# Kernel optimization log

Measured on AMD Instinct MI355X. Metric: run time of the kernel, lower is better.

Reference implementation:

```python
import jax, jax.numpy as jnp
import numpy as np

N, E, H, PIN, PEIN, POUT, L = 50000, 800000, 128, 16, 8, 8, 4
EPS = 1e-7


def setup_inputs() -> dict:
    key = jax.random.key(0)
    ks = jax.random.split(key, 24)
    f = jax.random.normal
    inp = {
        'x': f(ks[0], (N, PIN), jnp.float32),
        'edge_attr': f(ks[1], (E, PEIN), jnp.float32),
        'edge_index': jax.random.randint(ks[2], (2, E), 0, N, jnp.int32),
        # encoders
        'node_W': f(ks[3], (PIN, H)) * (1.0 / np.sqrt(PIN)),
        'node_b': jnp.zeros((H,)),
        'edge_W': f(ks[4], (PEIN, H)) * (1.0 / np.sqrt(PEIN)),
        'edge_b': jnp.zeros((H,)),
        # GENConv params per layer (stacked over L): MLP Linear(H,2H)->LN->ReLU->Linear(2H,H), temp t
        'W1': f(ks[5], (L, H, 2 * H)) * (1.0 / np.sqrt(H)),
        'b1': jnp.zeros((L, 2 * H)),
        'g1': jnp.ones((L, 2 * H)),
        'be1': jnp.zeros((L, 2 * H)),
        'W2': f(ks[6], (L, 2 * H, H)) * (1.0 / np.sqrt(2 * H)),
        'b2': jnp.zeros((L, H)),
        't': jnp.ones((L,)),
        # DeepGCNLayer LayerNorms
        'ng': jnp.ones((L, H)),
        'nb': jnp.zeros((L, H)),
        # output head
        'out_W': f(ks[7], (H, POUT)) * (1.0 / np.sqrt(H)),
        'out_b': jnp.zeros((POUT,)),
    }
    return inp


def _layernorm(x, g, b):
    mu = jnp.mean(x, -1, keepdims=True)
    v = jnp.mean(jnp.square(x - mu), -1, keepdims=True)
    return (x - mu) * jax.lax.rsqrt(v + 1e-5) * g + b


def reference(x, edge_attr, edge_index, node_W, node_b, edge_W, edge_b,
              W1, b1, g1, be1, W2, b2, t, ng, nb, out_W, out_b):
    src, dst = edge_index[0], edge_index[1]

    def genconv(h, e, i):
        # message: relu(x_j + edge_attr) + eps   [E, H]
        msg = jax.nn.relu(h[src] + e) + EPS
        # softmax aggregation over edges per destination node, temperature t[i]
        s = msg * t[i]
        m = jax.ops.segment_max(s, dst, num_segments=N)  # [N, H]
        w = jnp.exp(s - m[dst])
        denom = jax.ops.segment_sum(w, dst, num_segments=N)
        agg = jax.ops.segment_sum(msg * w, dst, num_segments=N)
        agg = jnp.where(denom > 0, agg / jnp.maximum(denom, EPS), 0.0)
        # root add, then 2-layer MLP (Linear -> LN -> ReLU -> Linear)
        z = agg + h
        z = jax.nn.relu(_layernorm(z @ W1[i] + b1[i], g1[i], be1[i]))
        return z @ W2[i] + b2[i]

    h = x @ node_W + node_b                      # node encoder
    e = jax.nn.sigmoid(edge_attr @ edge_W + edge_b)  # edge encoder
    h = genconv(h, e, 0)                         # layers[0].conv only
    for i in range(1, L):                        # res+ blocks
        z = jax.nn.relu(_layernorm(h, ng[i], nb[i]))
        h = h + genconv(z, e, i)
    h = jax.nn.relu(_layernorm(h, ng[0], nb[0]))  # layers[0] norm+act; dropout=eval identity
    return h @ out_W + out_b
```

## Files before the change

### kernel.cpp

```cpp
#include <hip/hip_runtime.h>
#include <hip/hip_bf16.h>

#define NN 50000
#define NE 800000
#define HH 128
#define PIN_ 16
#define PEIN_ 8
#define POUT_ 8
#define LAYERS_ 4
#define EPSM 1e-7f

typedef __bf16 bf16x8 __attribute__((ext_vector_type(8)));
typedef float f32x4 __attribute__((ext_vector_type(4)));
typedef float f32x2 __attribute__((ext_vector_type(2)));

__device__ inline unsigned short f2bf(float f) {
  unsigned int u = __float_as_uint(f);
  u += 0x7FFFu + ((u >> 16) & 1u);
  return (unsigned short)(u >> 16);
}
__device__ inline unsigned int packbf(float lo, float hi) {
  return (unsigned int)f2bf(lo) | ((unsigned int)f2bf(hi) << 16);
}
__device__ inline float bflo(unsigned int p) { return __uint_as_float(p << 16); }
__device__ inline float bfhi(unsigned int p) { return __uint_as_float(p & 0xFFFF0000u); }
__device__ inline f32x2 unpk(unsigned int p) {
  return (f32x2){__uint_as_float(p << 16), __uint_as_float(p & 0xFFFF0000u)};
}


__global__ void count_deg_kernel(const int* __restrict__ dst, int* __restrict__ deg) {
  int i = blockIdx.x * blockDim.x + threadIdx.x;
  if (i < NE) atomicAdd(&deg[dst[i]], 1);
}

__global__ __launch_bounds__(1024) void scan_kernel(const int* __restrict__ deg,
                                                    int* __restrict__ row_ptr,
                                                    int* __restrict__ cursor, int n) {
  __shared__ int wsum[16];
  __shared__ int carry_s;
  int t = threadIdx.x;
  int lane = t & 63, wv = t >> 6;
  if (t == 0) carry_s = 0;
  __syncthreads();
  for (int base = 0; base < n; base += 1024) {
    int i = base + t;
    int v = (i < n) ? deg[i] : 0;
    int x = v;
#pragma unroll
    for (int off = 1; off < 64; off <<= 1) {
      int y = __shfl_up(x, off, 64);
      if (lane >= off) x += y;
    }
    if (lane == 63) wsum[wv] = x;
    __syncthreads();
    if (wv == 0 && lane < 16) {
      int s = wsum[lane];
#pragma unroll
      for (int off = 1; off < 16; off <<= 1) {
        int y = __shfl_up(s, off, 16);
        if (lane >= off) s += y;
      }
      wsum[lane] = s;
    }
    __syncthreads();
    int waveExcl = (wv > 0) ? wsum[wv - 1] : 0;
    int carry = carry_s;
    int excl = carry + waveExcl + x - v;
    if (i < n) { row_ptr[i] = excl; cursor[i] = excl; }
    __syncthreads();
    if (t == 1023) carry_s = carry + wsum[15];
    __syncthreads();
  }
  if (t == 0) row_ptr[n] = carry_s;
}

__global__ void scatter_kernel(const int* __restrict__ src, const int* __restrict__ dst,
                               int* __restrict__ cursor, int2* __restrict__ csr,
                               int* __restrict__ srcs) {
  int i = blockIdx.x * blockDim.x + threadIdx.x;
  if (i < NE) {
    int d = dst[i];
    int pos = atomicAdd(&cursor[d], 1);
    csr[pos] = make_int2(src[i], i);
    srcs[pos] = src[i];
  }
}


__global__ __launch_bounds__(256) void edge_enc_kernel(
    const int2* __restrict__ csr, const float* __restrict__ edge_attr,
    const float* __restrict__ edge_W, const float* __restrict__ edge_b,
    int cap, unsigned int* __restrict__ epk) {
  int wv = threadIdx.x >> 6, lane = threadIdx.x & 63;
  int p = blockIdx.x * 4 + wv;
  if (p >= cap) return;
  int2 se = csr[p];
  const float4* ea = (const float4*)(edge_attr + (size_t)se.y * PEIN_);
  float4 A = ea[0], B = ea[1];
  float acc0 = edge_b[lane], acc1 = edge_b[lane + 64];
#pragma unroll
  for (int k = 0; k < PEIN_; ++k) {
    float av = (k < 4) ? ((k == 0) ? A.x : (k == 1) ? A.y : (k == 2) ? A.z : A.w)
                       : ((k == 4) ? B.x : (k == 5) ? B.y : (k == 6) ? B.z : B.w);
    acc0 = fmaf(av, edge_W[k * HH + lane], acc0);
    acc1 = fmaf(av, edge_W[k * HH + lane + 64], acc1);
  }
  float e0 = __builtin_amdgcn_rcpf(1.f + __expf(-acc0));
  float e1 = __builtin_amdgcn_rcpf(1.f + __expf(-acc1));
  epk[(size_t)p * 64 + lane] = packbf(e0, e1);
}


__device__ __forceinline__ void estep(unsigned int ep, unsigned int zp, float t,
                                      f32x2& d, f32x2& a) {
  f32x2 msg = unpk(zp) + unpk(ep);
  msg = __builtin_elementwise_max(msg, (f32x2){0.f, 0.f});
  msg += (f32x2){EPSM, EPSM};
  f32x2 s = msg * t;
  f32x2 w;
  w.x = __expf(s.x);
  w.y = __expf(s.y);
  d += w;
  a = __builtin_elementwise_fma(msg, w, a);
}

__device__ __forceinline__ void edge_step(float4 A, float4 B, unsigned int zp,
                                          const f32x2* ew, f32x2 eb, float t,
                                          f32x2& d, f32x2& a) {
  f32x2 acc = eb;
  acc = __builtin_elementwise_fma((f32x2){A.x, A.x}, ew[0], acc);
  acc = __builtin_elementwise_fma((f32x2){A.y, A.y}, ew[1], acc);
  acc = __builtin_elementwise_fma((f32x2){A.z, A.z}, ew[2], acc);
  acc = __builtin_elementwise_fma((f32x2){A.w, A.w}, ew[3], acc);
  acc = __builtin_elementwise_fma((f32x2){B.x, B.x}, ew[4], acc);
  acc = __builtin_elementwise_fma((f32x2){B.y, B.y}, ew[5], acc);
  acc = __builtin_elementwise_fma((f32x2){B.z, B.z}, ew[6], acc);
  acc = __builtin_elementwise_fma((f32x2){B.w, B.w}, ew[7], acc);
  f32x2 e;
  e.x = __builtin_amdgcn_rcpf(1.f + __expf(-acc.x));
  e.y = __builtin_amdgcn_rcpf(1.f + __expf(-acc.y));
  f32x2 msg = unpk(zp) + e;
  msg = __builtin_elementwise_max(msg, (f32x2){0.f, 0.f});
  msg += (f32x2){EPSM, EPSM};
  f32x2 s = msg * t;
  f32x2 w;
  w.x = __expf(s.x);
  w.y = __expf(s.y);
  d += w;
  a = __builtin_elementwise_fma(msg, w, a);
}

__global__ __launch_bounds__(256) void aggregate_hyb_kernel(
    const int* __restrict__ row_ptr, const int2* __restrict__ csr,
    const int* __restrict__ srcs, const unsigned int* __restrict__ epk, int cap,
    const float* __restrict__ edge_attr, const float* __restrict__ edge_W,
    const float* __restrict__ edge_b, const unsigned int* __restrict__ zpk,
    const float* __restrict__ t_all, int layer, unsigned int* __restrict__ upk) {
  int wv = threadIdx.x >> 6, lane = threadIdx.x & 63;
  int n = blockIdx.x * 4 + wv;
  if (n >= NN) return;
  float t = t_all[layer];
  int beg = row_ptr[n], end = row_ptr[n + 1];
  unsigned int zs = zpk[(size_t)n * 64 + lane];
  f32x2 d = {0.f, 0.f}, a = {0.f, 0.f};

  if (end <= cap) {
    int p = beg;
    for (; p + 4 <= end; p += 4) {
      int s0 = srcs[p], s1 = srcs[p + 1], s2 = srcs[p + 2], s3 = srcs[p + 3];
      unsigned int e0 = epk[(size_t)(p + 0) * 64 + lane];
      unsigned int e1 = epk[(size_t)(p + 1) * 64 + lane];
      unsigned int e2 = epk[(size_t)(p + 2) * 64 + lane];
      unsigned int e3 = epk[(size_t)(p + 3) * 64 + lane];
      unsigned int z0 = zpk[(size_t)s0 * 64 + lane];
      unsigned int z1 = zpk[(size_t)s1 * 64 + lane];
      unsigned int z2 = zpk[(size_t)s2 * 64 + lane];
      unsigned int z3 = zpk[(size_t)s3 * 64 + lane];
      estep(e0, z0, t, d, a);
      estep(e1, z1, t, d, a);
      estep(e2, z2, t, d, a);
      estep(e3, z3, t, d, a);
    }
    for (; p < end; ++p) {
      unsigned int e = epk[(size_t)p * 64 + lane];
      unsigned int z = zpk[(size_t)srcs[p] * 64 + lane];
      estep(e, z, t, d, a);
    }
  } else {
    f32x2 ew[PEIN_];
#pragma unroll
    for (int k = 0; k < PEIN_; ++k)
      ew[k] = (f32x2){edge_W[k * HH + lane], edge_W[k * HH + lane + 64]};
    f32x2 eb = (f32x2){edge_b[lane], edge_b[lane + 64]};
    int p = beg;
    for (; p + 4 <= end; p += 4) {
      int2 se0 = csr[p + 0];
      int2 se1 = csr[p + 1];
      int2 se2 = csr[p + 2];
      int2 se3 = csr[p + 3];
      const float4* e0p = (const float4*)(edge_attr + (size_t)se0.y * PEIN_);
      const float4* e1p = (const float4*)(edge_attr + (size_t)se1.y * PEIN_);
      const float4* e2p = (const float4*)(edge_attr + (size_t)se2.y * PEIN_);
      const float4* e3p = (const float4*)(edge_attr + (size_t)se3.y * PEIN_);
      float4 A0 = e0p[0], B0 = e0p[1];
      float4 A1 = e1p[0], B1 = e1p[1];
      float4 A2 = e2p[0], B2 = e2p[1];
      float4 A3 = e3p[0], B3 = e3p[1];
      unsigned int z0 = zpk[(size_t)se0.x * 64 + lane];
      unsigned int z1 = zpk[(size_t)se1.x * 64 + lane];
      unsigned int z2 = zpk[(size_t)se2.x * 64 + lane];
      unsigned int z3 = zpk[(size_t)se3.x * 64 + lane];
      edge_step(A0, B0, z0, ew, eb, t, d, a);
      edge_step(A1, B1, z1, ew, eb, t, d, a);
      edge_step(A2, B2, z2, ew, eb, t, d, a);
      edge_step(A3, B3, z3, ew, eb, t, d, a);
    }
    for (; p < end; ++p) {
      int2 se = csr[p];
      const float4* ep = (const float4*)(edge_attr + (size_t)se.y * PEIN_);
      float4 A = ep[0], B = ep[1];
      unsigned int zp = zpk[(size_t)se.x * 64 + lane];
      edge_step(A, B, zp, ew, eb, t, d, a);
    }
  }

  float agg0 = (d.x > 0.f) ? a.x / fmaxf(d.x, EPSM) : 0.f;
  float agg1 = (d.y > 0.f) ? a.y / fmaxf(d.y, EPSM) : 0.f;
  upk[(size_t)n * 64 + lane] = packbf(agg0 + bflo(zs), agg1 + bfhi(zs));
}


__global__ __launch_bounds__(256) void prep_weights_kernel(
    const float* __restrict__ W1, const float* __restrict__ W2,
    unsigned short* __restrict__ W1Tp, unsigned short* __restrict__ W2T) {
  int idx = blockIdx.x * 256 + threadIdx.x;
  if (idx >= LAYERS_ * 256 * 128) return;
  int l = idx >> 15, r = idx & 32767;
  int n = r >> 7, p = r & 127;
  int k = (p >> 1) + ((p & 1) << 6);
  W1Tp[idx] = f2bf(W1[(l << 15) + k * 256 + n]);
  int c = r >> 8, kk = r & 255;
  W2T[idx] = f2bf(W2[(l << 15) + kk * 128 + c]);
}


__global__ __launch_bounds__(64) void node_enc_kernel(const float* __restrict__ x,
                                                      const float* __restrict__ W,
                                                      const float* __restrict__ b,
                                                      unsigned int* __restrict__ hbp) {
  __shared__ float xs[8 * PIN_];
  int f = threadIdx.x;
  float w0[PIN_], w1[PIN_];
#pragma unroll
  for (int k = 0; k < PIN_; ++k) {
    w0[k] = W[k * HH + f];
    w1[k] = W[k * HH + f + 64];
  }
  float b0 = b[f], b1c = b[f + 64];
  int base = blockIdx.x * 8;
  xs[f] = x[(size_t)base * PIN_ + f];
  xs[f + 64] = x[(size_t)base * PIN_ + f + 64];
  __syncthreads();
#pragma unroll
  for (int r = 0; r < 8; ++r) {
    float a0 = b0, a1 = b1c;
#pragma unroll
    for (int k = 0; k < PIN_; ++k) {
      a0 = fmaf(xs[r * PIN_ + k], w0[k], a0);
      a1 = fmaf(xs[r * PIN_ + k], w1[k], a1);
    }
    hbp[(size_t)(base + r) * 64 + f] = packbf(a0, a1);
  }
}


__global__ __launch_bounds__(256) void mlp_fused_kernel(
    const unsigned int* __restrict__ upk,
    const unsigned short* __restrict__ W1Tp,
    const float* __restrict__ b1v, const float* __restrict__ g1v,
    const float* __restrict__ be1v,
    const unsigned short* __restrict__ W2T,
    const float* __restrict__ b2v,
    const float* __restrict__ res,
    const float* __restrict__ ngv, const float* __restrict__ nbv,
    float* __restrict__ hout, unsigned int* __restrict__ zbp) {
  __shared__ __align__(16) unsigned short Tlds[4 * 4096];
  int wv = threadIdx.x >> 6, lane = threadIdx.x & 63;
  int gw = blockIdx.x * 4 + wv;
  if (gw >= NN / 16) return;
  int row0 = gw * 16;
  int l15 = lane & 15, qg = lane >> 4;
  int co = 4 * qg;
  int sx = (l15 & 7) << 3;
  unsigned short* tl = Tlds + wv * 4096;

  const unsigned short* ub =
      (const unsigned short*)upk + (size_t)(row0 + l15) * HH + qg * 8;
  bf16x8 ufr[4];
#pragma unroll
  for (int kb = 0; kb < 4; ++kb) ufr[kb] = *(const bf16x8*)(ub + kb * 32);
  f32x4 acc1[16];
#pragma unroll
  for (int nb = 0; nb < 16; ++nb) acc1[nb] = (f32x4){0.f, 0.f, 0.f, 0.f};
#pragma unroll
  for (int nb = 0; nb < 16; ++nb) {
#pragma unroll
    for (int kb = 0; kb < 4; ++kb) {
      bf16x8 wf = *(const bf16x8*)(W1Tp + (size_t)(nb * 16 + l15) * HH + kb * 32 + qg * 8);
      acc1[nb] = __builtin_amdgcn_mfma_f32_16x16x32_bf16(wf, ufr[kb], acc1[nb], 0, 0, 0);
    }
  }

  float sum1 = 0.f;
#pragma unroll
  for (int nb = 0; nb < 16; ++nb) {
    float4 bq = *(const float4*)(b1v + nb * 16 + co);
    acc1[nb][0] += bq.x; acc1[nb][1] += bq.y;
    acc1[nb][2] += bq.z; acc1[nb][3] += bq.w;
    sum1 += acc1[nb][0] + acc1[nb][1] + acc1[nb][2] + acc1[nb][3];
  }
  sum1 += __shfl_xor(sum1, 16, 64);
  sum1 += __shfl_xor(sum1, 32, 64);
  float mu1 = sum1 * (1.f / 256.f);
  float sq1 = 0.f;
#pragma unroll
  for (int nb = 0; nb < 16; ++nb)
#pragma unroll
    for (int i = 0; i < 4; ++i) {
      float dd = acc1[nb][i] - mu1;
      sq1 = fmaf(dd, dd, sq1);
    }
  sq1 += __shfl_xor(sq1, 16, 64);
  sq1 += __shfl_xor(sq1, 32, 64);
  float rstd1 = rsqrtf(sq1 * (1.f / 256.f) + 1e-5f);
#pragma unroll
  for (int nb = 0; nb < 16; ++nb) {
    float4 gq = *(const float4*)(g1v + nb * 16 + co);
    float4 eq = *(const float4*)(be1v + nb * 16 + co);
    float t0 = fmaxf(fmaf((acc1[nb][0] - mu1) * rstd1, gq.x, eq.x), 0.f);
    float t1 = fmaxf(fmaf((acc1[nb][1] - mu1) * rstd1, gq.y, eq.y), 0.f);
    float t2 = fmaxf(fmaf((acc1[nb][2] - mu1) * rstd1, gq.z, eq.z), 0.f);
    float t3 = fmaxf(fmaf((acc1[nb][3] - mu1) * rstd1, gq.w, eq.w), 0.f);
    int ad = l15 * 256 + ((nb * 16 + co) ^ sx);
    *(uint2*)(tl + ad) = make_uint2(packbf(t0, t1), packbf(t2, t3));
  }

  f32x4 acc2[8];
#pragma unroll
  for (int nc = 0; nc < 8; ++nc) acc2[nc] = (f32x4){0.f, 0.f, 0.f, 0.f};
#pragma unroll
  for (int kb = 0; kb < 8; ++kb) {
    bf16x8 tf = *(const bf16x8*)(tl + l15 * 256 + ((kb * 32 + qg * 8) ^ sx));
#pragma unroll
    for (int nc = 0; nc < 8; ++nc) {
      bf16x8 wf = *(const bf16x8*)(W2T + (size_t)(nc * 16 + l15) * 256 + kb * 32 + qg * 8);
      acc2[nc] = __builtin_amdgcn_mfma_f32_16x16x32_bf16(wf, tf, acc2[nc], 0, 0, 0);
    }
  }

  size_t rb = (size_t)(row0 + l15) * HH;
  float sum2 = 0.f;
#pragma unroll
  for (int nc = 0; nc < 8; ++nc) {
    float4 bq = *(const float4*)(b2v + nc * 16 + co);
    acc2[nc][0] += bq.x; acc2[nc][1] += bq.y;
    acc2[nc][2] += bq.z; acc2[nc][3] += bq.w;
    if (res) {
      float4 rq = *(const float4*)(res + rb + nc * 16 + co);
      acc2[nc][0] += rq.x; acc2[nc][1] += rq.y;
      acc2[nc][2] += rq.z; acc2[nc][3] += rq.w;
    }
    *(float4*)(hout + rb + nc * 16 + co) =
        make_float4(acc2[nc][0], acc2[nc][1], acc2[nc][2], acc2[nc][3]);
    sum2 += acc2[nc][0] + acc2[nc][1] + acc2[nc][2] + acc2[nc][3];
  }
  sum2 += __shfl_xor(sum2, 16, 64);
  sum2 += __shfl_xor(sum2, 32, 64);
  float mu2 = sum2 * (1.f / 128.f);
  float sq2 = 0.f;
#pragma unroll
  for (int nc = 0; nc < 8; ++nc)
#pragma unroll
    for (int i = 0; i < 4; ++i) {
      float dd = acc2[nc][i] - mu2;
      sq2 = fmaf(dd, dd, sq2);
    }
  sq2 += __shfl_xor(sq2, 16, 64);
  sq2 += __shfl_xor(sq2, 32, 64);
  float rstd2 = rsqrtf(sq2 * (1.f / 128.f) + 1e-5f);
#pragma unroll
  for (int nc = 0; nc < 8; ++nc) {
    float4 gq = *(const float4*)(ngv + nc * 16 + co);
    float4 eq = *(const float4*)(nbv + nc * 16 + co);
    acc2[nc][0] = fmaxf(fmaf((acc2[nc][0] - mu2) * rstd2, gq.x, eq.x), 0.f);
    acc2[nc][1] = fmaxf(fmaf((acc2[nc][1] - mu2) * rstd2, gq.y, eq.y), 0.f);
    acc2[nc][2] = fmaxf(fmaf((acc2[nc][2] - mu2) * rstd2, gq.z, eq.z), 0.f);
    acc2[nc][3] = fmaxf(fmaf((acc2[nc][3] - mu2) * rstd2, gq.w, eq.w), 0.f);
  }
#pragma unroll
  for (int nc = 0; nc < 4; ++nc) {
    *(uint4*)(zbp + (size_t)(row0 + l15) * 64 + nc * 16 + co) =
        make_uint4(packbf(acc2[nc][0], acc2[nc + 4][0]),
                   packbf(acc2[nc][1], acc2[nc + 4][1]),
                   packbf(acc2[nc][2], acc2[nc + 4][2]),
                   packbf(acc2[nc][3], acc2[nc + 4][3]));
  }
}


__global__ __launch_bounds__(256) void out_head_kernel(const unsigned int* __restrict__ zbp,
                                                       const float* __restrict__ W,
                                                       const float* __restrict__ b,
                                                       float* __restrict__ out) {
  __shared__ float Wl[HH * POUT_];
  int t = threadIdx.x;
  for (int i = t; i < HH * POUT_; i += 256) Wl[i] = W[i];
  __syncthreads();
  int n = blockIdx.x * 32 + (t >> 3);
  int p = t & 7;
  if (n >= NN) return;
  float acc = b[p];
  const unsigned int* zr = zbp + (size_t)n * 64;
#pragma unroll 8
  for (int f = 0; f < 64; ++f) {
    unsigned int zp = zr[f];
    acc = fmaf(__uint_as_float(zp << 16), Wl[f * POUT_ + p], acc);
    acc = fmaf(__uint_as_float(zp & 0xFFFF0000u), Wl[(f + 64) * POUT_ + p], acc);
  }
  out[(size_t)n * POUT_ + p] = acc;
}


extern "C" void kernel_launch(void* const* d_in, const int* in_sizes, int n_in,
                              void* d_out, int out_size, void* d_ws, size_t ws_size,
                              hipStream_t stream) {
  const float* x = (const float*)d_in[0];
  const float* edge_attr = (const float*)d_in[1];
  const int* edge_index = (const int*)d_in[2];
  const float* node_W = (const float*)d_in[3];
  const float* node_b = (const float*)d_in[4];
  const float* edge_W = (const float*)d_in[5];
  const float* edge_b = (const float*)d_in[6];
  const float* W1 = (const float*)d_in[7];
  const float* b1 = (const float*)d_in[8];
  const float* g1 = (const float*)d_in[9];
  const float* be1 = (const float*)d_in[10];
  const float* W2 = (const float*)d_in[11];
  const float* b2 = (const float*)d_in[12];
  const float* t_all = (const float*)d_in[13];
  const float* ng = (const float*)d_in[14];
  const float* nb = (const float*)d_in[15];
  const float* out_W = (const float*)d_in[16];
  const float* out_b = (const float*)d_in[17];

  const int* src = edge_index;
  const int* dst = edge_index + NE;

  char* w = (char*)d_ws;
  float* h = (float*)w;
  unsigned int* upk = (unsigned int*)(w + 25600000);
  unsigned int* zbp = (unsigned int*)(w + 38400000);
  int* deg = (int*)(w + 51200000);
  int* row_ptr = (int*)(w + 51404800);
  int* cursor = (int*)(w + 51609600);
  int2* csr = (int2*)(w + 51814400);
  unsigned short* W1Tp = (unsigned short*)(w + 58214400);
  unsigned short* W2Tb = (unsigned short*)(w + 58476544);
  int* srcs = (int*)(w + 58738688);
  unsigned int* epk = (unsigned int*)(w + 61939200);

  long long avail = (long long)ws_size - 61939200ll;
  int cap = 0;
  if (avail > 0) {
    long long c = avail / 256;
    cap = (int)(c < (long long)NE ? c : (long long)NE);
  }

  hipMemsetAsync(deg, 0, NN * sizeof(int), stream);
  count_deg_kernel<<<(NE + 255) / 256, 256, 0, stream>>>(dst, deg);
  scan_kernel<<<1, 1024, 0, stream>>>(deg, row_ptr, cursor, NN);
  scatter_kernel<<<(NE + 255) / 256, 256, 0, stream>>>(src, dst, cursor, csr, srcs);
  if (cap > 0)
    edge_enc_kernel<<<(cap + 3) / 4, 256, 0, stream>>>(csr, edge_attr, edge_W, edge_b,
                                                       cap, epk);
  prep_weights_kernel<<<512, 256, 0, stream>>>(W1, W2, W1Tp, W2Tb);
  node_enc_kernel<<<NN / 8, 64, 0, stream>>>(x, node_W, node_b, zbp);

  const int mlp_blocks = (NN / 16 + 3) / 4;
  for (int i = 0; i < LAYERS_; ++i) {
    aggregate_hyb_kernel<<<NN / 4, 256, 0, stream>>>(row_ptr, csr, srcs, epk, cap,
                                                     edge_attr, edge_W, edge_b,
                                                     zbp, t_all, i, upk);
    int zn = (i + 1) % LAYERS_;
    mlp_fused_kernel<<<mlp_blocks, 256, 0, stream>>>(
        upk, W1Tp + (size_t)i * 32768, b1 + i * 256, g1 + i * 256, be1 + i * 256,
        W2Tb + (size_t)i * 32768, b2 + i * HH,
        (i == 0) ? nullptr : h,
        ng + zn * HH, nb + zn * HH, h, zbp);
  }
  out_head_kernel<<<(NN + 31) / 32, 256, 0, stream>>>(zbp, out_W, out_b, (float*)d_out);
}
```

Before: 1.047 ms.

## Recompute edge encoding in aggregation and build CSR via atomic offsets

Drops the precomputed bf16 edge-encoding buffer (edge_enc_kernel) and always recomputes sigmoid(edge_attr@edge_W) inside each aggregation layer from the 32-byte raw attributes. CSR construction now records each edge's slot from the degree-count atomic and places edges without a second atomic pass or cursor array. The aim is to cut the 256 bytes per edge of encoded-edge traffic read each layer, plus one setup kernel, at the cost of an 8-FMA matvec and an extra exp per edge per layer.

```diff
diff --git a/kernel.cpp b/kernel.cpp
--- a/kernel.cpp
+++ b/kernel.cpp
@@ -29,14 +29,14 @@
 }
 
 
-__global__ void count_deg_kernel(const int* __restrict__ dst, int* __restrict__ deg) {
+__global__ void count_deg_kernel(const int* __restrict__ dst, int* __restrict__ deg,
+                                 int* __restrict__ kof) {
   int i = blockIdx.x * blockDim.x + threadIdx.x;
-  if (i < NE) atomicAdd(&deg[dst[i]], 1);
+  if (i < NE) kof[i] = atomicAdd(&deg[dst[i]], 1);
 }
 
 __global__ __launch_bounds__(1024) void scan_kernel(const int* __restrict__ deg,
-                                                    int* __restrict__ row_ptr,
-                                                    int* __restrict__ cursor, int n) {
+                                                    int* __restrict__ row_ptr, int n) {
   __shared__ int wsum[16];
   __shared__ int carry_s;
   int t = threadIdx.x;
@@ -67,7 +67,7 @@
     int waveExcl = (wv > 0) ? wsum[wv - 1] : 0;
     int carry = carry_s;
     int excl = carry + waveExcl + x - v;
-    if (i < n) { row_ptr[i] = excl; cursor[i] = excl; }
+    if (i < n) row_ptr[i] = excl;
     __syncthreads();
     if (t == 1023) carry_s = carry + wsum[15];
     __syncthreads();
@@ -75,55 +75,16 @@
   if (t == 0) row_ptr[n] = carry_s;
 }
 
-__global__ void scatter_kernel(const int* __restrict__ src, const int* __restrict__ dst,
-                               int* __restrict__ cursor, int2* __restrict__ csr,
-                               int* __restrict__ srcs) {
+__global__ void place_kernel(const int* __restrict__ src, const int* __restrict__ dst,
+                             const int* __restrict__ row_ptr, const int* __restrict__ kof,
+                             int2* __restrict__ csr) {
   int i = blockIdx.x * blockDim.x + threadIdx.x;
   if (i < NE) {
-    int d = dst[i];
-    int pos = atomicAdd(&cursor[d], 1);
+    int pos = row_ptr[dst[i]] + kof[i];
     csr[pos] = make_int2(src[i], i);
-    srcs[pos] = src[i];
-  }
-}
-
-
-__global__ __launch_bounds__(256) void edge_enc_kernel(
-    const int2* __restrict__ csr, const float* __restrict__ edge_attr,
-    const float* __restrict__ edge_W, const float* __restrict__ edge_b,
-    int cap, unsigned int* __restrict__ epk) {
-  int wv = threadIdx.x >> 6, lane = threadIdx.x & 63;
-  int p = blockIdx.x * 4 + wv;
-  if (p >= cap) return;
-  int2 se = csr[p];
-  const float4* ea = (const float4*)(edge_attr + (size_t)se.y * PEIN_);
-  float4 A = ea[0], B = ea[1];
-  float acc0 = edge_b[lane], acc1 = edge_b[lane + 64];
-#pragma unroll
-  for (int k = 0; k < PEIN_; ++k) {
-    float av = (k < 4) ? ((k == 0) ? A.x : (k == 1) ? A.y : (k == 2) ? A.z : A.w)
-                       : ((k == 4) ? B.x : (k == 5) ? B.y : (k == 6) ? B.z : B.w);
-    acc0 = fmaf(av, edge_W[k * HH + lane], acc0);
-    acc1 = fmaf(av, edge_W[k * HH + lane + 64], acc1);
-  }
-  float e0 = __builtin_amdgcn_rcpf(1.f + __expf(-acc0));
-  float e1 = __builtin_amdgcn_rcpf(1.f + __expf(-acc1));
-  epk[(size_t)p * 64 + lane] = packbf(e0, e1);
-}
-
-
-__device__ __forceinline__ void estep(unsigned int ep, unsigned int zp, float t,
-                                      f32x2& d, f32x2& a) {
-  f32x2 msg = unpk(zp) + unpk(ep);
-  msg = __builtin_elementwise_max(msg, (f32x2){0.f, 0.f});
-  msg += (f32x2){EPSM, EPSM};
-  f32x2 s = msg * t;
-  f32x2 w;
-  w.x = __expf(s.x);
-  w.y = __expf(s.y);
-  d += w;
-  a = __builtin_elementwise_fma(msg, w, a);
-}
+  }
+}
+
 
 __device__ __forceinline__ void edge_step(float4 A, float4 B, unsigned int zp,
                                           const f32x2* ew, f32x2 eb, float t,
@@ -151,80 +112,53 @@
   a = __builtin_elementwise_fma(msg, w, a);
 }
 
-__global__ __launch_bounds__(256) void aggregate_hyb_kernel(
+__global__ __launch_bounds__(256) void aggregate_kernel(
     const int* __restrict__ row_ptr, const int2* __restrict__ csr,
-    const int* __restrict__ srcs, const unsigned int* __restrict__ epk, int cap,
     const float* __restrict__ edge_attr, const float* __restrict__ edge_W,
     const float* __restrict__ edge_b, const unsigned int* __restrict__ zpk,
     const float* __restrict__ t_all, int layer, unsigned int* __restrict__ upk) {
   int wv = threadIdx.x >> 6, lane = threadIdx.x & 63;
   int n = blockIdx.x * 4 + wv;
   if (n >= NN) return;
+  f32x2 ew[PEIN_];
+#pragma unroll
+  for (int k = 0; k < PEIN_; ++k)
+    ew[k] = (f32x2){edge_W[k * HH + lane], edge_W[k * HH + lane + 64]};
+  f32x2 eb = (f32x2){edge_b[lane], edge_b[lane + 64]};
   float t = t_all[layer];
   int beg = row_ptr[n], end = row_ptr[n + 1];
   unsigned int zs = zpk[(size_t)n * 64 + lane];
   f32x2 d = {0.f, 0.f}, a = {0.f, 0.f};
-
-  if (end <= cap) {
-    int p = beg;
-    for (; p + 4 <= end; p += 4) {
-      int s0 = srcs[p], s1 = srcs[p + 1], s2 = srcs[p + 2], s3 = srcs[p + 3];
-      unsigned int e0 = epk[(size_t)(p + 0) * 64 + lane];
-      unsigned int e1 = epk[(size_t)(p + 1) * 64 + lane];
-      unsigned int e2 = epk[(size_t)(p + 2) * 64 + lane];
-      unsigned int e3 = epk[(size_t)(p + 3) * 64 + lane];
-      unsigned int z0 = zpk[(size_t)s0 * 64 + lane];
-      unsigned int z1 = zpk[(size_t)s1 * 64 + lane];
-      unsigned int z2 = zpk[(size_t)s2 * 64 + lane];
-      unsigned int z3 = zpk[(size_t)s3 * 64 + lane];
-      estep(e0, z0, t, d, a);
-      estep(e1, z1, t, d, a);
-      estep(e2, z2, t, d, a);
-      estep(e3, z3, t, d, a);
-    }
-    for (; p < end; ++p) {
-      unsigned int e = epk[(size_t)p * 64 + lane];
-      unsigned int z = zpk[(size_t)srcs[p] * 64 + lane];
-      estep(e, z, t, d, a);
-    }
-  } else {
-    f32x2 ew[PEIN_];
-#pragma unroll
-    for (int k = 0; k < PEIN_; ++k)
-      ew[k] = (f32x2){edge_W[k * HH + lane], edge_W[k * HH + lane + 64]};
-    f32x2 eb = (f32x2){edge_b[lane], edge_b[lane + 64]};
-    int p = beg;
-    for (; p + 4 <= end; p += 4) {
-      int2 se0 = csr[p + 0];
-      int2 se1 = csr[p + 1];
-      int2 se2 = csr[p + 2];
-      int2 se3 = csr[p + 3];
-      const float4* e0p = (const float4*)(edge_attr + (size_t)se0.y * PEIN_);
-      const float4* e1p = (const float4*)(edge_attr + (size_t)se1.y * PEIN_);
-      const float4* e2p = (const float4*)(edge_attr + (size_t)se2.y * PEIN_);
-      const float4* e3p = (const float4*)(edge_attr + (size_t)se3.y * PEIN_);
-      float4 A0 = e0p[0], B0 = e0p[1];
-      float4 A1 = e1p[0], B1 = e1p[1];
-      float4 A2 = e2p[0], B2 = e2p[1];
-      float4 A3 = e3p[0], B3 = e3p[1];
-      unsigned int z0 = zpk[(size_t)se0.x * 64 + lane];
-      unsigned int z1 = zpk[(size_t)se1.x * 64 + lane];
-      unsigned int z2 = zpk[(size_t)se2.x * 64 + lane];
-      unsigned int z3 = zpk[(size_t)se3.x * 64 + lane];
-      edge_step(A0, B0, z0, ew, eb, t, d, a);
-      edge_step(A1, B1, z1, ew, eb, t, d, a);
-      edge_step(A2, B2, z2, ew, eb, t, d, a);
-      edge_step(A3, B3, z3, ew, eb, t, d, a);
-    }
-    for (; p < end; ++p) {
-      int2 se = csr[p];
-      const float4* ep = (const float4*)(edge_attr + (size_t)se.y * PEIN_);
-      float4 A = ep[0], B = ep[1];
-      unsigned int zp = zpk[(size_t)se.x * 64 + lane];
-      edge_step(A, B, zp, ew, eb, t, d, a);
-    }
-  }
-
+  int p = beg;
+  for (; p + 4 <= end; p += 4) {
+    int2 se0 = csr[p + 0];
+    int2 se1 = csr[p + 1];
+    int2 se2 = csr[p + 2];
+    int2 se3 = csr[p + 3];
+    const float4* e0p = (const float4*)(edge_attr + (size_t)se0.y * PEIN_);
+    const float4* e1p = (const float4*)(edge_attr + (size_t)se1.y * PEIN_);
+    const float4* e2p = (const float4*)(edge_attr + (size_t)se2.y * PEIN_);
+    const float4* e3p = (const float4*)(edge_attr + (size_t)se3.y * PEIN_);
+    float4 A0 = e0p[0], B0 = e0p[1];
+    float4 A1 = e1p[0], B1 = e1p[1];
+    float4 A2 = e2p[0], B2 = e2p[1];
+    float4 A3 = e3p[0], B3 = e3p[1];
+    unsigned int z0 = zpk[(size_t)se0.x * 64 + lane];
+    unsigned int z1 = zpk[(size_t)se1.x * 64 + lane];
+    unsigned int z2 = zpk[(size_t)se2.x * 64 + lane];
+    unsigned int z3 = zpk[(size_t)se3.x * 64 + lane];
+    edge_step(A0, B0, z0, ew, eb, t, d, a);
+    edge_step(A1, B1, z1, ew, eb, t, d, a);
+    edge_step(A2, B2, z2, ew, eb, t, d, a);
+    edge_step(A3, B3, z3, ew, eb, t, d, a);
+  }
+  for (; p < end; ++p) {
+    int2 se = csr[p];
+    const float4* ep = (const float4*)(edge_attr + (size_t)se.y * PEIN_);
+    float4 A = ep[0], B = ep[1];
+    unsigned int zp = zpk[(size_t)se.x * 64 + lane];
+    edge_step(A, B, zp, ew, eb, t, d, a);
+  }
   float agg0 = (d.x > 0.f) ? a.x / fmaxf(d.x, EPSM) : 0.f;
   float agg1 = (d.y > 0.f) ? a.y / fmaxf(d.y, EPSM) : 0.f;
   upk[(size_t)n * 64 + lane] = packbf(agg0 + bflo(zs), agg1 + bfhi(zs));
@@ -463,35 +397,22 @@
   unsigned int* zbp = (unsigned int*)(w + 38400000);
   int* deg = (int*)(w + 51200000);
   int* row_ptr = (int*)(w + 51404800);
-  int* cursor = (int*)(w + 51609600);
-  int2* csr = (int2*)(w + 51814400);
-  unsigned short* W1Tp = (unsigned short*)(w + 58214400);
-  unsigned short* W2Tb = (unsigned short*)(w + 58476544);
-  int* srcs = (int*)(w + 58738688);
-  unsigned int* epk = (unsigned int*)(w + 61939200);
-
-  long long avail = (long long)ws_size - 61939200ll;
-  int cap = 0;
-  if (avail > 0) {
-    long long c = avail / 256;
-    cap = (int)(c < (long long)NE ? c : (long long)NE);
-  }
+  int2* csr = (int2*)(w + 51609600);
+  unsigned short* W1Tp = (unsigned short*)(w + 58009600);
+  unsigned short* W2Tb = (unsigned short*)(w + 58271744);
+  int* kof = (int*)(w + 58533888);
 
   hipMemsetAsync(deg, 0, NN * sizeof(int), stream);
-  count_deg_kernel<<<(NE + 255) / 256, 256, 0, stream>>>(dst, deg);
-  scan_kernel<<<1, 1024, 0, stream>>>(deg, row_ptr, cursor, NN);
-  scatter_kernel<<<(NE + 255) / 256, 256, 0, stream>>>(src, dst, cursor, csr, srcs);
-  if (cap > 0)
-    edge_enc_kernel<<<(cap + 3) / 4, 256, 0, stream>>>(csr, edge_attr, edge_W, edge_b,
-                                                       cap, epk);
+  count_deg_kernel<<<(NE + 255) / 256, 256, 0, stream>>>(dst, deg, kof);
+  scan_kernel<<<1, 1024, 0, stream>>>(deg, row_ptr, NN);
+  place_kernel<<<(NE + 255) / 256, 256, 0, stream>>>(src, dst, row_ptr, kof, csr);
   prep_weights_kernel<<<512, 256, 0, stream>>>(W1, W2, W1Tp, W2Tb);
   node_enc_kernel<<<NN / 8, 64, 0, stream>>>(x, node_W, node_b, zbp);
 
   const int mlp_blocks = (NN / 16 + 3) / 4;
   for (int i = 0; i < LAYERS_; ++i) {
-    aggregate_hyb_kernel<<<NN / 4, 256, 0, stream>>>(row_ptr, csr, srcs, epk, cap,
-                                                     edge_attr, edge_W, edge_b,
-                                                     zbp, t_all, i, upk);
+    aggregate_kernel<<<NN / 4, 256, 0, stream>>>(row_ptr, csr, edge_attr, edge_W,
+                                                 edge_b, zbp, t_all, i, upk);
     int zn = (i + 1) % LAYERS_;
     mlp_fused_kernel<<<mlp_blocks, 256, 0, stream>>>(
         upk, W1Tp + (size_t)i * 32768, b1 + i * 256, g1 + i * 256, be1 + i * 256,
```

After: 899.0 us. 1.16x faster.
